# Kernel tuning notes

Measured on AMD Instinct MI355X. Metric: run time of the kernel, lower is better.

## Reference

```python
import jax, jax.numpy as jnp
import numpy as np

TAU = 2.0      # LIF membrane time constant
VTH = 1.0      # spike threshold
ALPHA = 2.0    # surrogate-gradient sharpness (atan surrogate)
EPS = 1e-5     # BatchNorm eps

@jax.custom_vjp
def spike(u):
    return (u > 0.0).astype(u.dtype)

def _spike_fwd(u):
    return spike(u), u

def _spike_bwd(u, g):
    sg = ALPHA / (2.0 * (1.0 + (jnp.pi / 2.0 * ALPHA * u) ** 2))
    return (g * sg,)

spike.defvjp(_spike_fwd, _spike_bwd)

def lif_time(x):
    # x: [B,T,C,H,W] -> spikes [B,T,C,H,W]; hard-reset LIF, v0 = 0
    xT = jnp.moveaxis(x, 1, 0)  # [T,B,C,H,W]
    def step(v, xt):
        v = v + (xt - v) / TAU
        s = spike(v - VTH)
        return v * (1.0 - s), s
    _, sT = jax.lax.scan(step, jnp.zeros_like(xT[0]), xT)
    return jnp.moveaxis(sT, 0, 1)

def conv2d(x, w, stride, pad):
    return jax.lax.conv_general_dilated(
        x, w, (stride, stride), [(pad, pad), (pad, pad)],
        dimension_numbers=('NCHW', 'OIHW', 'NCHW'))

def bn(x, gamma, beta, mean, var):
    # inference-style BatchNorm2d with running stats; x: [N,C,H,W]
    inv = gamma * jax.lax.rsqrt(var + EPS)
    return x * inv[None, :, None, None] + (beta - mean * inv)[None, :, None, None]

def setup_inputs() -> dict:
    key = jax.random.key(0)
    ks = jax.random.split(key, 16)
    B, T, Cin, Cout, H, W = 16, 8, 128, 256, 56, 56
    d = {}
    d['x_spike'] = (jax.random.uniform(ks[0], (B, T, Cin, H, W)) < 0.2).astype(jnp.float32)
    d['conv1_w'] = jax.random.normal(ks[1], (Cout, Cin, 3, 3), dtype=jnp.float32) * 0.05
    d['conv2_w'] = jax.random.normal(ks[2], (Cout, Cout, 3, 3), dtype=jnp.float32) * 0.05
    d['ds_w'] = jax.random.normal(ks[3], (Cout, Cin, 1, 1), dtype=jnp.float32) * 0.05
    for i, p in enumerate(['n1', 'n2', 'nd']):
        d[p + '_gamma'] = 1.0 + 0.1 * jax.random.normal(ks[4 + i], (Cout,), dtype=jnp.float32)
        d[p + '_beta'] = 0.1 * jax.random.normal(ks[7 + i], (Cout,), dtype=jnp.float32)
        d[p + '_mean'] = 0.01 * jax.random.normal(ks[10 + i], (Cout,), dtype=jnp.float32)
        d[p + '_var'] = jax.random.uniform(ks[13 + i], (Cout,), minval=0.5, maxval=1.5)
    return d

def reference(x_spike, conv1_w, conv2_w, ds_w,
              n1_gamma, n1_beta, n1_mean, n1_var,
              n2_gamma, n2_beta, n2_mean, n2_var,
              nd_gamma, nd_beta, nd_mean, nd_var):
    B, T, Cin, H, W = x_spike.shape
    x_flat = x_spike.reshape(B * T, Cin, H, W)
    # downsample shortcut (1x1 conv stride 2 + BN)
    identity = bn(conv2d(x_flat, ds_w, 2, 0), nd_gamma, nd_beta, nd_mean, nd_var)
    # NOTE: original module runs lif_shortcut on identity but DISCARDS the result
    # (pure state side-effect); it does not affect the output, so it is omitted.
    out = bn(conv2d(x_flat, conv1_w, 2, 1), n1_gamma, n1_beta, n1_mean, n1_var)
    Cout, Ho, Wo = out.shape[1], out.shape[2], out.shape[3]
    out = lif_time(out.reshape(B, T, Cout, Ho, Wo))
    out = bn(conv2d(out.reshape(B * T, Cout, Ho, Wo), conv2_w, 1, 1),
             n2_gamma, n2_beta, n2_mean, n2_var) + identity
    return lif_time(out.reshape(B, T, Cout, Ho, Wo))
```

## Files before the change

### kernel.cpp

```cpp
#include <hip/hip_runtime.h>
#include <hip/hip_bf16.h>

#define CIN  128
#define CO   256
#define HIN  56
#define WIN  56
#define OH   28
#define OWW  28
#define P    784
#define HWIN 3136
#define PERT 200704

typedef __attribute__((ext_vector_type(8))) short bf16x8v;
typedef __attribute__((ext_vector_type(4))) float f32x4;

__device__ __forceinline__ f32x4 mfma16(bf16x8v a, bf16x8v b, f32x4 c) {
    return __builtin_amdgcn_mfma_f32_16x16x32_bf16(a, b, c, 0, 0, 0);
}

__device__ __forceinline__ void gld_lds16(const void* g, void* l) {
    __builtin_amdgcn_global_load_lds(
        (const __attribute__((address_space(1))) void*)g,
        (__attribute__((address_space(3))) void*)l, 16, 0, 0);
}

__global__ __launch_bounds__(256) void k_prep_bias(
    const float* __restrict__ g1, const float* __restrict__ b1,
    const float* __restrict__ m1, const float* __restrict__ v1,
    const float* __restrict__ g2, const float* __restrict__ b2,
    const float* __restrict__ m2, const float* __restrict__ v2,
    const float* __restrict__ gd, const float* __restrict__ bd,
    const float* __restrict__ md, const float* __restrict__ vd,
    float* __restrict__ inv1o, float* __restrict__ bias1o,
    float* __restrict__ inv2o, float* __restrict__ invdo,
    float* __restrict__ bias2o)
{
    int co = threadIdx.x;
    float inv1 = g1[co] / sqrtf(v1[co] + 1e-5f);
    float inv2 = g2[co] / sqrtf(v2[co] + 1e-5f);
    float invd = gd[co] / sqrtf(vd[co] + 1e-5f);
    inv1o[co]  = inv1;
    bias1o[co] = fmaf(-m1[co], inv1, b1[co]);
    inv2o[co]  = inv2;
    invdo[co]  = invd;
    bias2o[co] = fmaf(-m2[co], inv2, b2[co]) + fmaf(-md[co], invd, bd[co]);
}

__global__ __launch_bounds__(256) void k_prep_w2p(
    const float* __restrict__ w2, const float* __restrict__ inv2,
    unsigned short* __restrict__ hi, unsigned short* __restrict__ lo)
{
    int i = blockIdx.x * 256 + threadIdx.x;
    if (i >= 73728) return;
    int tap = i >> 13;
    int r   = i & 8191;
    int ch  = r >> 10;
    int r2  = r & 1023;
    int cf  = r2 >> 6;
    int lane = r2 & 63;
    int co  = cf * 16 + (lane & 15);
    int cib = ch * 32 + (lane >> 4) * 8;
#pragma unroll
    for (int j = 0; j < 8; j++) {
        float w = w2[((size_t)co * CO + cib + j) * 9 + tap] * inv2[co];
        __hip_bfloat16 h = __float2bfloat16(w);
        __hip_bfloat16 l = __float2bfloat16(w - __bfloat162float(h));
        hi[(size_t)i * 8 + j] = *(unsigned short*)&h;
        lo[(size_t)i * 8 + j] = *(unsigned short*)&l;
    }
}

__global__ __launch_bounds__(256) void k_prep_w1p(
    const float* __restrict__ w1, const float* __restrict__ inv1,
    unsigned short* __restrict__ hi, unsigned short* __restrict__ mid,
    unsigned short* __restrict__ lo)
{
    int i = blockIdx.x * 256 + threadIdx.x;
    if (i >= 36864) return;
    int tap = i >> 12;
    int r   = i & 4095;
    int ch  = r >> 10;
    int r2  = r & 1023;
    int cf  = r2 >> 6;
    int lane = r2 & 63;
    int co  = cf * 16 + (lane & 15);
    int cib = ch * 32 + (lane >> 4) * 8;
#pragma unroll
    for (int j = 0; j < 8; j++) {
        float w = w1[((size_t)co * CIN + cib + j) * 9 + tap] * inv1[co];
        __hip_bfloat16 h = __float2bfloat16(w);
        float r1 = w - __bfloat162float(h);
        __hip_bfloat16 m = __float2bfloat16(r1);
        float r2f = r1 - __bfloat162float(m);
        __hip_bfloat16 l = __float2bfloat16(r2f);
        hi[(size_t)i * 8 + j]  = *(unsigned short*)&h;
        mid[(size_t)i * 8 + j] = *(unsigned short*)&m;
        lo[(size_t)i * 8 + j]  = *(unsigned short*)&l;
    }
}

__global__ __launch_bounds__(256) void k_prep_wdp(
    const float* __restrict__ wd, const float* __restrict__ invd,
    unsigned short* __restrict__ hi, unsigned short* __restrict__ lo)
{
    int i = blockIdx.x * 256 + threadIdx.x;
    if (i >= 4096) return;
    int ch  = i >> 10;
    int r2  = i & 1023;
    int cf  = r2 >> 6;
    int lane = r2 & 63;
    int co  = cf * 16 + (lane & 15);
    int cib = ch * 32 + (lane >> 4) * 8;
#pragma unroll
    for (int j = 0; j < 8; j++) {
        float w = wd[(size_t)co * CIN + cib + j] * invd[co];
        __hip_bfloat16 h = __float2bfloat16(w);
        __hip_bfloat16 l = __float2bfloat16(w - __bfloat162float(h));
        hi[(size_t)i * 8 + j] = *(unsigned short*)&h;
        lo[(size_t)i * 8 + j] = *(unsigned short*)&l;
    }
}

__global__ __launch_bounds__(256) void k_pack1(
    const float* __restrict__ x, unsigned int* __restrict__ xt_p)
{
    int i = blockIdx.x * 256 + threadIdx.x;
    int pos = i % HWIN;
    int nw  = i / HWIN;
    int w   = nw & 3;
    int n   = nw >> 2;
    const float* xp = x + ((size_t)n * CIN + w * 32) * HWIN + pos;
    unsigned int word = 0;
#pragma unroll
    for (int ci = 0; ci < 32; ci++)
        if (xp[(size_t)ci * HWIN] != 0.f) word |= (1u << ci);
    xt_p[((size_t)n * HWIN + pos) * 4 + w] = word;
}

__global__ __launch_bounds__(256) void k_conv1_mfma(
    const unsigned int* __restrict__ xt_p,
    const unsigned short* __restrict__ w1hip,
    const unsigned short* __restrict__ w1midp,
    const unsigned short* __restrict__ w1lop,
    const float* __restrict__ bias1,
    float* __restrict__ out)
{
    __shared__ unsigned int XW[4 * 522];

    const int n    = blockIdx.x / 7;
    const int rt   = blockIdx.x - n * 7;
    const int r0   = rt * 4;
    const int tid  = threadIdx.x;
    const int wave = tid >> 6;
    const int lane = tid & 63;
    const int l15  = lane & 15;
    const int quad = lane >> 4;
    const int cf0  = blockIdx.y * 8 + wave * 2;

    const unsigned int* xp_n = xt_p + (size_t)n * HWIN * 4;
    for (int i = tid; i < 513; i += 256) {
        int row = i / 57, c = i - row * 57;
        int irow = 2 * r0 - 1 + row;
        int iw   = c - 1;
        uint4 val = {0u, 0u, 0u, 0u};
        if (irow >= 0 && iw >= 0)
            val = *(const uint4*)(xp_n + (size_t)(irow * WIN + iw) * 4);
        int base = row * 58 + c;
        XW[0 * 522 + base] = val.x;
        XW[1 * 522 + base] = val.y;
        XW[2 * 522 + base] = val.z;
        XW[3 * 522 + base] = val.w;
    }
    __syncthreads();

    int rr[7], cc[7];
#pragma unroll
    for (int f = 0; f < 7; f++) {
        int pos = f * 16 + l15;
        rr[f] = pos / 28;
        cc[f] = pos - rr[f] * 28;
    }

    f32x4 acc[2][7];
#pragma unroll
    for (int g = 0; g < 2; g++)
#pragma unroll
        for (int f = 0; f < 7; f++) acc[g][f] = (f32x4){0.f, 0.f, 0.f, 0.f};

    bf16x8v ch0, cm0, cl0, ch1, cm1, cl1;
    bf16x8v nh0, nm0, nl0, nh1, nm1, nl1;
    {
        size_t b0 = ((size_t)0 * 16 + cf0) * 512 + lane * 8;
        ch0 = *(const bf16x8v*)(w1hip + b0);  cm0 = *(const bf16x8v*)(w1midp + b0);
        cl0 = *(const bf16x8v*)(w1lop + b0);
        ch1 = *(const bf16x8v*)(w1hip + b0 + 512); cm1 = *(const bf16x8v*)(w1midp + b0 + 512);
        cl1 = *(const bf16x8v*)(w1lop + b0 + 512);
        nh0 = ch0; nm0 = cm0; nl0 = cl0; nh1 = ch1; nm1 = cm1; nl1 = cl1;
    }

    for (int c = 0; c < 4; c++) {
        for (int tap = 0; tap < 9; tap++) {
            int rd = c * 9 + tap;
            if (rd < 35) {
                int rn = rd + 1, cn = rn / 9, tn = rn - cn * 9;
                size_t b0 = ((size_t)(tn * 4 + cn) * 16 + cf0) * 512 + lane * 8;
                nh0 = *(const bf16x8v*)(w1hip + b0);  nm0 = *(const bf16x8v*)(w1midp + b0);
                nl0 = *(const bf16x8v*)(w1lop + b0);
                nh1 = *(const bf16x8v*)(w1hip + b0 + 512); nm1 = *(const bf16x8v*)(w1midp + b0 + 512);
                nl1 = *(const bf16x8v*)(w1lop + b0 + 512);
            }
            const int kh = tap / 3, kw = tap - kh * 3;
#pragma unroll
            for (int f = 0; f < 7; f++) {
                unsigned int word = XW[c * 522 + (2 * rr[f] + kh) * 58 + 2 * cc[f] + kw];
                unsigned int byt  = (word >> (quad * 8)) & 0xffu;
                uint4 u;
                u.x = ((byt & 1u)   ? 0x3F80u : 0u) | ((byt & 2u)   ? 0x3F800000u : 0u);
                u.y = ((byt & 4u)   ? 0x3F80u : 0u) | ((byt & 8u)   ? 0x3F800000u : 0u);
                u.z = ((byt & 16u)  ? 0x3F80u : 0u) | ((byt & 32u)  ? 0x3F800000u : 0u);
                u.w = ((byt & 64u)  ? 0x3F80u : 0u) | ((byt & 128u) ? 0x3F800000u : 0u);
                union { uint4 q; bf16x8v v; } cv;
                cv.q = u;
                acc[0][f] = mfma16(ch0, cv.v, acc[0][f]);
                acc[0][f] = mfma16(cm0, cv.v, acc[0][f]);
                acc[0][f] = mfma16(cl0, cv.v, acc[0][f]);
                acc[1][f] = mfma16(ch1, cv.v, acc[1][f]);
                acc[1][f] = mfma16(cm1, cv.v, acc[1][f]);
                acc[1][f] = mfma16(cl1, cv.v, acc[1][f]);
            }
            ch0 = nh0; cm0 = nm0; cl0 = nl0; ch1 = nh1; cm1 = nm1; cl1 = nl1;
        }
    }

#pragma unroll
    for (int g = 0; g < 2; g++)
#pragma unroll
        for (int f = 0; f < 7; f++) {
            int pg = rt * 112 + f * 16 + l15;
#pragma unroll
            for (int reg = 0; reg < 4; reg++) {
                int co = cf0 * 16 + g * 16 + quad * 4 + reg;
                out[((size_t)n * CO + co) * P + pg] = acc[g][f][reg] + bias1[co];
            }
        }
}

__global__ __launch_bounds__(256) void k_lif1t(
    const float* __restrict__ pre, unsigned short* __restrict__ st)
{
    __shared__ unsigned short T[16 * 68];
    const int b   = blockIdx.x;
    const int co0 = blockIdx.y * 64;
    const int p0  = blockIdx.z * 16;
    const int tid  = threadIdx.x;
    const int pcol = tid & 15;
    const int g    = tid >> 4;
    const int pos = p0 + g;
    const int oh  = pos / 28, ow = pos - oh * 28;
    const int f8  = ((((oh + 1) * 30 + ow + 1) >> 1) & 3);
    const int o      = (pcol & 7) >> 1;
    const int no     = o ^ f8;
    const int within = (pcol & 1) * 4;
    const int chp    = (co0 >> 5) + (pcol >> 3);
    float v[4] = {0.f, 0.f, 0.f, 0.f};
    for (int t = 0; t < 8; t++) {
        const float* src = pre + (((size_t)(b * 8 + t)) * CO + co0) * P + p0;
        unsigned short s[4];
#pragma unroll
        for (int j = 0; j < 4; j++) {
            int co = g + 16 * j;
            float xv = src[(size_t)co * P + pcol];
            v[j] = v[j] + (xv - v[j]) * 0.5f;
            bool sp = v[j] > 1.0f;
            s[j] = sp ? 0x3F80 : 0;
            if (sp) v[j] = 0.f;
        }
        __syncthreads();
#pragma unroll
        for (int j = 0; j < 4; j++) T[pcol * 68 + g + 16 * j] = s[j];
        __syncthreads();
        unsigned short* dst = st + (((size_t)(b * 8 + t) * 8 + chp) * P + pos) * 32
                               + no * 8 + within;
        ushort4 ov;
        ov.x = T[g * 68 + pcol * 4 + 0];
        ov.y = T[g * 68 + pcol * 4 + 1];
        ov.z = T[g * 68 + pcol * 4 + 2];
        ov.w = T[g * 68 + pcol * 4 + 3];
        *(ushort4*)dst = ov;
    }
}

__global__ __launch_bounds__(256) void k_conv2_mfma(
    const unsigned short* __restrict__ spike_t,
    const unsigned int* __restrict__ xt_p,
    const unsigned short* __restrict__ w2hip,
    const unsigned short* __restrict__ w2lop,
    const unsigned short* __restrict__ wdhip,
    const unsigned short* __restrict__ wdlop,
    const float* __restrict__ bias2,
    float* __restrict__ out)
{
    __shared__ unsigned short SB[2 * 5760];
    __shared__ unsigned int   XW2[4 * 112];

    const int n    = blockIdx.x / 7;
    const int rt   = blockIdx.x - n * 7;
    const int r0   = rt * 4;
    const int tid  = threadIdx.x;
    const int wave = tid >> 6;
    const int lane = tid & 63;
    const int l15  = lane & 15;
    const int quad = lane >> 4;
    const int cf0  = wave * 4;

    {
        uint4 z = {0u, 0u, 0u, 0u};
        for (int i = tid; i < 1440; i += 256) ((uint4*)SB)[i] = z;
    }
    for (int i = tid; i < 112; i += 256) {
        int r = i / 28, c = i - r * 28;
        uint4 w4 = *(const uint4*)(xt_p + ((size_t)n * HWIN
                    + (2 * (r0 + r)) * WIN + 2 * c) * 4);
        XW2[0 * 112 + i] = w4.x;
        XW2[1 * 112 + i] = w4.y;
        XW2[2 * 112 + i] = w4.z;
        XW2[3 * 112 + i] = w4.w;
    }
    __syncthreads();

    int  g_irow[3], g_lds[3];
    bool g_ok[3];
    int  g_half[3];
#pragma unroll
    for (int k = 0; k < 3; k++) {
        int idx  = wave * 3 + k;
        int row  = idx >> 1, half = idx & 1;
        int irow = r0 - 1 + row;
        g_irow[k] = irow;
        g_half[k] = half;
        g_ok[k]   = ((unsigned)irow < 28u) && (half == 0 || lane < 48);
        g_lds[k]  = row * 1920 + 64 + half * 1024;
    }
    const char* sp_n = (const char*)spike_t + (size_t)n * 8 * P * 64;

#pragma unroll
    for (int k = 0; k < 3; k++)
        if (g_ok[k])
            gld_lds16(sp_n + (size_t)g_irow[k] * 1792 + g_half[k] * 1024 + lane * 16,
                      (char*)SB + g_lds[k]);

    int rr[7], cc[7];
#pragma unroll
    for (int f = 0; f < 7; f++) {
        int pos = f * 16 + l15;
        rr[f] = pos / 28;
        cc[f] = pos - rr[f] * 28;
    }

    f32x4 acc[4][7];
#pragma unroll
    for (int g = 0; g < 4; g++)
#pragma unroll
        for (int f = 0; f < 7; f++) acc[g][f] = (f32x4){0.f, 0.f, 0.f, 0.f};

    for (int c = 0; c < 4; c++) {
        size_t b0 = ((size_t)c * 16 + cf0) * 512 + lane * 8;
        bf16x8v ah[4], al[4];
#pragma unroll
        for (int g = 0; g < 4; g++) {
            ah[g] = *(const bf16x8v*)(wdhip + b0 + g * 512);
            al[g] = *(const bf16x8v*)(wdlop + b0 + g * 512);
        }
#pragma unroll
        for (int f = 0; f < 7; f++) {
            unsigned int word = XW2[c * 112 + rr[f] * 28 + cc[f]];
            unsigned int byt  = (word >> (quad * 8)) & 0xffu;
            uint4 u;
            u.x = ((byt & 1u)   ? 0x3F80u : 0u) | ((byt & 2u)   ? 0x3F800000u : 0u);
            u.y = ((byt & 4u)   ? 0x3F80u : 0u) | ((byt & 8u)   ? 0x3F800000u : 0u);
            u.z = ((byt & 16u)  ? 0x3F80u : 0u) | ((byt & 32u)  ? 0x3F800000u : 0u);
            u.w = ((byt & 64u)  ? 0x3F80u : 0u) | ((byt & 128u) ? 0x3F800000u : 0u);
            union { uint4 q; bf16x8v v; } cv;
            cv.q = u;
#pragma unroll
            for (int g = 0; g < 4; g++) {
                acc[g][f] = mfma16(ah[g], cv.v, acc[g][f]);
                acc[g][f] = mfma16(al[g], cv.v, acc[g][f]);
            }
        }
    }
    __syncthreads();

    bf16x8v cw[8], nx[8];
    {
        size_t b0 = ((size_t)0 * 16 + cf0) * 512 + lane * 8;
#pragma unroll
        for (int g = 0; g < 4; g++) {
            cw[2 * g]     = *(const bf16x8v*)(w2hip + b0 + g * 512);
            cw[2 * g + 1] = *(const bf16x8v*)(w2lop + b0 + g * 512);
            nx[2 * g]     = cw[2 * g];
            nx[2 * g + 1] = cw[2 * g + 1];
        }
    }

    for (int c = 0; c < 8; c++) {
        if (c < 7) {
            const char* base = sp_n + (size_t)(c + 1) * 50176;
            char* dstb = (char*)SB + ((c + 1) & 1) * 11520;
#pragma unroll
            for (int k = 0; k < 3; k++)
                if (g_ok[k])
                    gld_lds16(base + (size_t)g_irow[k] * 1792 + g_half[k] * 1024 + lane * 16,
                              dstb + g_lds[k]);
        }
        const int bufsh = (c & 1) * 5760;
        for (int tap = 0; tap < 9; tap++) {
            int rd = c * 9 + tap;
            if (rd < 71) {
                int rn = rd + 1, cn = rn / 9, tn = rn - cn * 9;
                size_t b0 = ((size_t)(tn * 8 + cn) * 16 + cf0) * 512 + lane * 8;
#pragma unroll
                for (int g = 0; g < 4; g++) {
                    nx[2 * g]     = *(const bf16x8v*)(w2hip + b0 + g * 512);
                    nx[2 * g + 1] = *(const bf16x8v*)(w2lop + b0 + g * 512);
                }
            }
            const int kh = tap / 3, kw = tap - kh * 3;
#pragma unroll
            for (int f = 0; f < 7; f++) {
                int slot = (rr[f] + kh) * 30 + cc[f] + kw;
                int sw   = (slot >> 1) & 3;
                bf16x8v bfr = *(const bf16x8v*)(
                    &SB[bufsh + slot * 32 + ((quad ^ sw) * 8)]);
#pragma unroll
                for (int g = 0; g < 4; g++) {
                    acc[g][f] = mfma16(cw[2 * g], bfr, acc[g][f]);
                    acc[g][f] = mfma16(cw[2 * g + 1], bfr, acc[g][f]);
                }
            }
#pragma unroll
            for (int j = 0; j < 8; j++) cw[j] = nx[j];
        }
        __syncthreads();
    }

#pragma unroll
    for (int g = 0; g < 4; g++)
#pragma unroll
        for (int f = 0; f < 7; f++) {
            int pg = rt * 112 + f * 16 + l15;
#pragma unroll
            for (int reg = 0; reg < 4; reg++) {
                int co = (cf0 + g) * 16 + quad * 4 + reg;
                out[((size_t)n * CO + co) * P + pg] = acc[g][f][reg] + bias2[co];
            }
        }
}

__global__ __launch_bounds__(256) void k_lif4(const float4* __restrict__ in,
                                              float4* __restrict__ out)
{
    const int q = PERT / 4;
    const int i = blockIdx.x * 256 + threadIdx.x;
    const int b = i / q;
    const int r = i - b * q;
    const float4* pi = in  + (size_t)(b * 8) * q + r;
    float4*       po = out + (size_t)(b * 8) * q + r;
    float v0 = 0.f, v1 = 0.f, v2 = 0.f, v3 = 0.f;
#pragma unroll
    for (int t = 0; t < 8; t++) {
        float4 xt = pi[(size_t)t * q];
        float4 s;
        v0 = v0 + (xt.x - v0) * 0.5f; s.x = (v0 > 1.0f) ? 1.f : 0.f; if (v0 > 1.0f) v0 = 0.f;
        v1 = v1 + (xt.y - v1) * 0.5f; s.y = (v1 > 1.0f) ? 1.f : 0.f; if (v1 > 1.0f) v1 = 0.f;
        v2 = v2 + (xt.z - v2) * 0.5f; s.z = (v2 > 1.0f) ? 1.f : 0.f; if (v2 > 1.0f) v2 = 0.f;
        v3 = v3 + (xt.w - v3) * 0.5f; s.w = (v3 > 1.0f) ? 1.f : 0.f; if (v3 > 1.0f) v3 = 0.f;
        po[(size_t)t * q] = s;
    }
}

extern "C" void kernel_launch(void* const* d_in, const int* in_sizes, int n_in,
                              void* d_out, int out_size, void* d_ws, size_t ws_size,
                              hipStream_t stream) {
    const float* x   = (const float*)d_in[0];
    const float* w1  = (const float*)d_in[1];
    const float* w2  = (const float*)d_in[2];
    const float* wd  = (const float*)d_in[3];
    const float* n1g = (const float*)d_in[4];
    const float* n1b = (const float*)d_in[5];
    const float* n1m = (const float*)d_in[6];
    const float* n1v = (const float*)d_in[7];
    const float* n2g = (const float*)d_in[8];
    const float* n2b = (const float*)d_in[9];
    const float* n2m = (const float*)d_in[10];
    const float* n2v = (const float*)d_in[11];
    const float* ndg = (const float*)d_in[12];
    const float* ndb = (const float*)d_in[13];
    const float* ndm = (const float*)d_in[14];
    const float* ndv = (const float*)d_in[15];

    float* out = (float*)d_out;

    char* w = (char*)d_ws;
    unsigned short* spike_t = (unsigned short*)w;
    unsigned short* w2hip   = (unsigned short*)(w + 51380224);
    unsigned short* w2lop   = (unsigned short*)(w + 52559872);
    unsigned short* w1hip   = (unsigned short*)(w + 53739520);
    unsigned short* w1midp  = (unsigned short*)(w + 54329344);
    unsigned short* w1lop   = (unsigned short*)(w + 54919168);
    unsigned short* wdhip   = (unsigned short*)(w + 55508992);
    unsigned short* wdlop   = (unsigned short*)(w + 55574528);
    float*          bias2   = (float*)(w + 55640064);
    float*          bias1   = (float*)(w + 55641088);
    float*          inv1    = (float*)(w + 55642112);
    float*          inv2    = (float*)(w + 55643136);
    float*          invd    = (float*)(w + 55644160);
    unsigned int*   xt_p    = (unsigned int*)(w + 55645184);

    k_prep_bias<<<1, 256, 0, stream>>>(n1g, n1b, n1m, n1v,
                                       n2g, n2b, n2m, n2v,
                                       ndg, ndb, ndm, ndv,
                                       inv1, bias1, inv2, invd, bias2);
    k_prep_w2p<<<288, 256, 0, stream>>>(w2, inv2, w2hip, w2lop);
    k_prep_w1p<<<144, 256, 0, stream>>>(w1, inv1, w1hip, w1midp, w1lop);
    k_prep_wdp<<<16, 256, 0, stream>>>(wd, invd, wdhip, wdlop);

    k_pack1<<<(128 * 4 * HWIN) / 256, 256, 0, stream>>>(x, xt_p);
    k_conv1_mfma<<<dim3(896, 2), 256, 0, stream>>>(
        xt_p, w1hip, w1midp, w1lop, bias1, out);
    k_lif1t<<<dim3(16, 4, 49), 256, 0, stream>>>(out, spike_t);
    k_conv2_mfma<<<dim3(896), 256, 0, stream>>>(
        spike_t, xt_p, w2hip, w2lop, wdhip, wdlop, bias2, out);
    k_lif4<<<(16 * (PERT / 4)) / 256, 256, 0, stream>>>(
        (const float4*)out, (float4*)out);
}
```

Measured before the change: 713.7 us.

## Cover all output channels per conv1 block, dropping the y-grid split

Result: no change. 722.2 us (+1.2%).

```diff
diff --git a/kernel.cpp b/kernel.cpp
--- a/kernel.cpp
+++ b/kernel.cpp
@@ -155,7 +155,7 @@
     const int lane = tid & 63;
     const int l15  = lane & 15;
     const int quad = lane >> 4;
-    const int cf0  = blockIdx.y * 8 + wave * 2;
+    const int cf0  = wave * 4;
 
     const unsigned int* xp_n = xt_p + (size_t)n * HWIN * 4;
     for (int i = tid; i < 513; i += 256) {
@@ -181,33 +181,21 @@
         cc[f] = pos - rr[f] * 28;
     }
 
-    f32x4 acc[2][7];
-#pragma unroll
-    for (int g = 0; g < 2; g++)
+    f32x4 acc[4][7];
+#pragma unroll
+    for (int g = 0; g < 4; g++)
 #pragma unroll
         for (int f = 0; f < 7; f++) acc[g][f] = (f32x4){0.f, 0.f, 0.f, 0.f};
-
-    bf16x8v ch0, cm0, cl0, ch1, cm1, cl1;
-    bf16x8v nh0, nm0, nl0, nh1, nm1, nl1;
-    {
-        size_t b0 = ((size_t)0 * 16 + cf0) * 512 + lane * 8;
-        ch0 = *(const bf16x8v*)(w1hip + b0);  cm0 = *(const bf16x8v*)(w1midp + b0);
-        cl0 = *(const bf16x8v*)(w1lop + b0);
-        ch1 = *(const bf16x8v*)(w1hip + b0 + 512); cm1 = *(const bf16x8v*)(w1midp + b0 + 512);
-        cl1 = *(const bf16x8v*)(w1lop + b0 + 512);
-        nh0 = ch0; nm0 = cm0; nl0 = cl0; nh1 = ch1; nm1 = cm1; nl1 = cl1;
-    }
 
     for (int c = 0; c < 4; c++) {
         for (int tap = 0; tap < 9; tap++) {
-            int rd = c * 9 + tap;
-            if (rd < 35) {
-                int rn = rd + 1, cn = rn / 9, tn = rn - cn * 9;
-                size_t b0 = ((size_t)(tn * 4 + cn) * 16 + cf0) * 512 + lane * 8;
-                nh0 = *(const bf16x8v*)(w1hip + b0);  nm0 = *(const bf16x8v*)(w1midp + b0);
-                nl0 = *(const bf16x8v*)(w1lop + b0);
-                nh1 = *(const bf16x8v*)(w1hip + b0 + 512); nm1 = *(const bf16x8v*)(w1midp + b0 + 512);
-                nl1 = *(const bf16x8v*)(w1lop + b0 + 512);
+            size_t b0 = ((size_t)(tap * 4 + c) * 16 + cf0) * 512 + lane * 8;
+            bf16x8v ah[4], am[4], al[4];
+#pragma unroll
+            for (int g = 0; g < 4; g++) {
+                ah[g] = *(const bf16x8v*)(w1hip  + b0 + g * 512);
+                am[g] = *(const bf16x8v*)(w1midp + b0 + g * 512);
+                al[g] = *(const bf16x8v*)(w1lop  + b0 + g * 512);
             }
             const int kh = tap / 3, kw = tap - kh * 3;
 #pragma unroll
@@ -221,25 +209,24 @@
                 u.w = ((byt & 64u)  ? 0x3F80u : 0u) | ((byt & 128u) ? 0x3F800000u : 0u);
                 union { uint4 q; bf16x8v v; } cv;
                 cv.q = u;
-                acc[0][f] = mfma16(ch0, cv.v, acc[0][f]);
-                acc[0][f] = mfma16(cm0, cv.v, acc[0][f]);
-                acc[0][f] = mfma16(cl0, cv.v, acc[0][f]);
-                acc[1][f] = mfma16(ch1, cv.v, acc[1][f]);
-                acc[1][f] = mfma16(cm1, cv.v, acc[1][f]);
-                acc[1][f] = mfma16(cl1, cv.v, acc[1][f]);
-            }
-            ch0 = nh0; cm0 = nm0; cl0 = nl0; ch1 = nh1; cm1 = nm1; cl1 = nl1;
-        }
-    }
-
-#pragma unroll
-    for (int g = 0; g < 2; g++)
+#pragma unroll
+                for (int g = 0; g < 4; g++) {
+                    acc[g][f] = mfma16(ah[g], cv.v, acc[g][f]);
+                    acc[g][f] = mfma16(am[g], cv.v, acc[g][f]);
+                    acc[g][f] = mfma16(al[g], cv.v, acc[g][f]);
+                }
+            }
+        }
+    }
+
+#pragma unroll
+    for (int g = 0; g < 4; g++)
 #pragma unroll
         for (int f = 0; f < 7; f++) {
             int pg = rt * 112 + f * 16 + l15;
 #pragma unroll
             for (int reg = 0; reg < 4; reg++) {
-                int co = cf0 * 16 + g * 16 + quad * 4 + reg;
+                int co = (cf0 + g) * 16 + quad * 4 + reg;
                 out[((size_t)n * CO + co) * P + pg] = acc[g][f][reg] + bias1[co];
             }
         }
@@ -526,7 +513,7 @@
     k_prep_wdp<<<16, 256, 0, stream>>>(wd, invd, wdhip, wdlop);
 
     k_pack1<<<(128 * 4 * HWIN) / 256, 256, 0, stream>>>(x, xt_p);
-    k_conv1_mfma<<<dim3(896, 2), 256, 0, stream>>>(
+    k_conv1_mfma<<<dim3(896), 256, 0, stream>>>(
         xt_p, w1hip, w1midp, w1lop, bias1, out);
     k_lif1t<<<dim3(16, 4, 49), 256, 0, stream>>>(out, spike_t);
     k_conv2_mfma<<<dim3(896), 256, 0, stream>>>(
```
